# Optimization experiments

Measured on AMD Instinct MI355X. Metric: run time of the kernel, lower is better.

## Reference

```python
import jax, jax.numpy as jnp
import numpy as np

B, S, RNN, ATTH = 256, 196, 1024, 512  # batch, att_size, rnn_size, att_h_size


def setup_inputs() -> dict:
    key = jax.random.key(0)
    k1, k2, k3, k4, k5, k6, k7 = jax.random.split(key, 7)
    h = jax.random.normal(k1, (B, RNN), dtype=jnp.float32)
    att_feats = jax.random.normal(k2, (B, S, RNN), dtype=jnp.float32)
    p_att_feats = jax.random.normal(k3, (B, S, ATTH), dtype=jnp.float32)
    # learned params (torch nn.Linear: y = x @ W.T + b)
    w_h2att = jax.random.normal(k4, (ATTH, RNN), dtype=jnp.float32) / np.sqrt(RNN)
    b_h2att = jax.random.normal(k5, (ATTH,), dtype=jnp.float32) * 0.01
    w_alpha = jax.random.normal(k6, (1, ATTH), dtype=jnp.float32) / np.sqrt(ATTH)
    b_alpha = jax.random.normal(k7, (1,), dtype=jnp.float32) * 0.01
    return {
        "h": h,
        "att_feats": att_feats,
        "p_att_feats": p_att_feats,
        "w_h2att": w_h2att,
        "b_h2att": b_h2att,
        "w_alpha": w_alpha,
        "b_alpha": b_alpha,
    }


def reference(h, att_feats, p_att_feats, w_h2att, b_h2att, w_alpha, b_alpha):
    # att_h = h2att(h): [B, ATTH]
    att_h = h @ w_h2att.T + b_h2att
    # additive combine + tanh: [B, S, ATTH]
    dot = jnp.tanh(p_att_feats + att_h[:, None, :])
    # alpha_net: [B, S]
    scores = jnp.einsum("bsa,a->bs", dot, w_alpha[0]) + b_alpha[0]
    weight = jax.nn.softmax(scores, axis=1)
    # weighted sum of att_feats: [B, RNN]
    att_res = jnp.einsum("bs,bsd->bd", weight, att_feats)
    return att_res
```

## Files before the change

kernel.cpp:

```cpp
#include <hip/hip_runtime.h>
#include <cstddef>

static constexpr int kB    = 256;
static constexpr int kS    = 196;
static constexpr int kRNN  = 1024;
static constexpr int kATTH = 512;

__device__ __forceinline__ float fast_tanh(float x) {
    x = fminf(12.0f, fmaxf(-12.0f, x));
    float e = __expf(2.0f * x);
    return __fdividef(e - 1.0f, e + 1.0f);
}

__device__ __forceinline__ float dot8t(const float4 p0, const float4 p1,
                                       const float4 ah0, const float4 ah1,
                                       const float4 wa0, const float4 wa1) {
    float r;
    r  = fast_tanh(p0.x + ah0.x) * wa0.x;
    r += fast_tanh(p0.y + ah0.y) * wa0.y;
    r += fast_tanh(p0.z + ah0.z) * wa0.z;
    r += fast_tanh(p0.w + ah0.w) * wa0.w;
    r += fast_tanh(p1.x + ah1.x) * wa1.x;
    r += fast_tanh(p1.y + ah1.y) * wa1.y;
    r += fast_tanh(p1.z + ah1.z) * wa1.z;
    r += fast_tanh(p1.w + ah1.w) * wa1.w;
    return r;
}

__global__ __launch_bounds__(1024) void att_one(
    const float* __restrict__ h,
    const float* __restrict__ att_feats,
    const float* __restrict__ p_att,
    const float* __restrict__ w_h2att,
    const float* __restrict__ b_h2att,
    const float* __restrict__ w_alpha,
    const float* __restrict__ b_alpha,
    float* __restrict__ out) {
    const int b = blockIdx.x;
    const int tid = threadIdx.x;
    const int lane = tid & 63;
    const int wave = tid >> 6;

    __shared__ float sAttH[kATTH];
    __shared__ float sScore[kS];
    __shared__ float4 sRed[3][256];

    {
        const float* hb = &h[(size_t)b * kRNN];
        const int k0 = lane << 2;
        const float4 h0 = *(const float4*)&hb[k0];
        const float4 h1 = *(const float4*)&hb[k0 + 256];
        const float4 h2 = *(const float4*)&hb[k0 + 512];
        const float4 h3 = *(const float4*)&hb[k0 + 768];
        const int abase = wave << 5;
#pragma unroll 2
        for (int r = 0; r < 32; ++r) {
            const int a = abase + r;
            const float* wr = &w_h2att[(size_t)a * kRNN + k0];
            const float4 x0 = *(const float4*)(wr);
            const float4 x1 = *(const float4*)(wr + 256);
            const float4 x2 = *(const float4*)(wr + 512);
            const float4 x3 = *(const float4*)(wr + 768);
            float d;
            d  = x0.x * h0.x + x0.y * h0.y + x0.z * h0.z + x0.w * h0.w;
            d += x1.x * h1.x + x1.y * h1.y + x1.z * h1.z + x1.w * h1.w;
            d += x2.x * h2.x + x2.y * h2.y + x2.z * h2.z + x2.w * h2.w;
            d += x3.x * h3.x + x3.y * h3.y + x3.z * h3.z + x3.w * h3.w;
#pragma unroll
            for (int off = 32; off > 0; off >>= 1) d += __shfl_xor(d, off, 64);
            if (lane == 0) sAttH[a] = d + b_h2att[a];
        }
    }
    __syncthreads();

    {
        const int col = lane << 3;
        const float4 ah0 = *(const float4*)&sAttH[col];
        const float4 ah1 = *(const float4*)&sAttH[col + 4];
        const float4 wa0 = *(const float4*)&w_alpha[col];
        const float4 wa1 = *(const float4*)&w_alpha[col + 4];
        const float balpha = b_alpha[0];

        for (int s = wave; s < kS; s += 32) {
            const int s2 = s + 16;
            const float* p = &p_att[((size_t)b * kS + s) * kATTH + col];
            const float4 p0 = *(const float4*)p;
            const float4 p1 = *(const float4*)(p + 4);
            float4 q0 = {0.f, 0.f, 0.f, 0.f}, q1 = {0.f, 0.f, 0.f, 0.f};
            if (s2 < kS) {
                const float* q = p + (size_t)16 * kATTH;
                q0 = *(const float4*)q;
                q1 = *(const float4*)(q + 4);
            }
            float r1 = dot8t(p0, p1, ah0, ah1, wa0, wa1);
#pragma unroll
            for (int off = 32; off > 0; off >>= 1) r1 += __shfl_xor(r1, off, 64);
            if (lane == 0) sScore[s] = r1 + balpha;
            if (s2 < kS) {
                float r2 = dot8t(q0, q1, ah0, ah1, wa0, wa1);
#pragma unroll
                for (int off = 32; off > 0; off >>= 1) r2 += __shfl_xor(r2, off, 64);
                if (lane == 0) sScore[s2] = r2 + balpha;
            }
        }
    }
    __syncthreads();

    if (tid < 64) {
        float vals[4];
        int cnt = 0;
        float m = -3.0e38f;
        for (int s = tid; s < kS; s += 64) {
            vals[cnt] = sScore[s];
            m = fmaxf(m, vals[cnt]);
            ++cnt;
        }
#pragma unroll
        for (int off = 32; off > 0; off >>= 1) m = fmaxf(m, __shfl_xor(m, off, 64));
        float sum = 0.f;
        for (int i = 0; i < cnt; ++i) { vals[i] = __expf(vals[i] - m); sum += vals[i]; }
#pragma unroll
        for (int off = 32; off > 0; off >>= 1) sum += __shfl_xor(sum, off, 64);
        const float inv = __fdividef(1.0f, sum);
        cnt = 0;
        for (int s = tid; s < kS; s += 64) { sScore[s] = vals[cnt] * inv; ++cnt; }
    }
    __syncthreads();

    const int d4 = tid & 255;
    const int sg = tid >> 8;
    const float* af = &att_feats[(size_t)b * kS * kRNN + (d4 << 2)];
    float4 acc = {0.f, 0.f, 0.f, 0.f};
#pragma unroll 4
    for (int i = 0; i < 49; ++i) {
        const int s = (i << 2) + sg;
        const float ws = sScore[s];
        const float4 v = *(const float4*)&af[(size_t)s * kRNN];
        acc.x += ws * v.x; acc.y += ws * v.y;
        acc.z += ws * v.z; acc.w += ws * v.w;
    }
    if (sg > 0) sRed[sg - 1][d4] = acc;
    __syncthreads();
    if (sg == 0) {
        const float4 r0 = sRed[0][d4];
        const float4 r1 = sRed[1][d4];
        const float4 r2 = sRed[2][d4];
        acc.x += r0.x + r1.x + r2.x;
        acc.y += r0.y + r1.y + r2.y;
        acc.z += r0.z + r1.z + r2.z;
        acc.w += r0.w + r1.w + r2.w;
        *(float4*)&out[(size_t)b * kRNN + (d4 << 2)] = acc;
    }
}

extern "C" void kernel_launch(void* const* d_in, const int* in_sizes, int n_in,
                              void* d_out, int out_size, void* d_ws, size_t ws_size,
                              hipStream_t stream) {
    const float* h         = (const float*)d_in[0];
    const float* att_feats = (const float*)d_in[1];
    const float* p_att     = (const float*)d_in[2];
    const float* w_h2att   = (const float*)d_in[3];
    const float* b_h2att   = (const float*)d_in[4];
    const float* w_alpha   = (const float*)d_in[5];
    const float* b_alpha   = (const float*)d_in[6];
    float* out = (float*)d_out;

    att_one<<<kB, 1024, 0, stream>>>(h, att_feats, p_att, w_h2att, b_h2att,
                                     w_alpha, b_alpha, out);
}
```

Measured before the change: 383.8 us.

## Fuse softmax and weighted sum into score loop using static max bound

Replaces the three-phase score/softmax/weighted-sum structure with one streaming loop per wave. Each wave computes a score, exponentiates it against a static upper bound (sum of |w_alpha| plus |b_alpha|, since tanh is bounded), and accumulates exp-weighted att_feats rows directly. Partial sums are then reduced across waves through shared memory. The p_att and att_feats loads for the first row are issued before the h2att GEMV, and the next row is prefetched each iteration. This removes two block barriers and the serial single-wave softmax, and overlaps memory loads with compute. The risks are that the fixed-bound exponent could underflow if scores sit far below the bound, and that the 64 KB shared accumulator array may limit occupancy.

```diff
diff --git a/kernel.cpp b/kernel.cpp
--- a/kernel.cpp
+++ b/kernel.cpp
@@ -42,8 +42,25 @@
     const int wave = tid >> 6;
 
     __shared__ float sAttH[kATTH];
-    __shared__ float sScore[kS];
-    __shared__ float4 sRed[3][256];
+    __shared__ float4 sAcc[16][256];
+    __shared__ float sSum[16];
+
+    const int col = lane << 3;
+    const float* pbase = &p_att[(size_t)b * kS * kATTH + col];
+    const float* abase = &att_feats[(size_t)b * kS * kRNN + (lane << 2)];
+
+    int s = wave;
+    float4 p0, p1, v0, v1, v2, v3;
+    {
+        const float* p = pbase + (size_t)s * kATTH;
+        p0 = *(const float4*)p;
+        p1 = *(const float4*)(p + 4);
+        const float* a = abase + (size_t)s * kRNN;
+        v0 = *(const float4*)(a);
+        v1 = *(const float4*)(a + 256);
+        v2 = *(const float4*)(a + 512);
+        v3 = *(const float4*)(a + 768);
+    }
 
     {
         const float* hb = &h[(size_t)b * kRNN];
@@ -52,10 +69,10 @@
         const float4 h1 = *(const float4*)&hb[k0 + 256];
         const float4 h2 = *(const float4*)&hb[k0 + 512];
         const float4 h3 = *(const float4*)&hb[k0 + 768];
-        const int abase = wave << 5;
+        const int abase0 = wave << 5;
 #pragma unroll 2
         for (int r = 0; r < 32; ++r) {
-            const int a = abase + r;
+            const int a = abase0 + r;
             const float* wr = &w_h2att[(size_t)a * kRNN + k0];
             const float4 x0 = *(const float4*)(wr);
             const float4 x1 = *(const float4*)(wr + 256);
@@ -73,84 +90,67 @@
     }
     __syncthreads();
 
-    {
-        const int col = lane << 3;
-        const float4 ah0 = *(const float4*)&sAttH[col];
-        const float4 ah1 = *(const float4*)&sAttH[col + 4];
-        const float4 wa0 = *(const float4*)&w_alpha[col];
-        const float4 wa1 = *(const float4*)&w_alpha[col + 4];
-        const float balpha = b_alpha[0];
+    const float4 ah0 = *(const float4*)&sAttH[col];
+    const float4 ah1 = *(const float4*)&sAttH[col + 4];
+    const float4 wa0 = *(const float4*)&w_alpha[col];
+    const float4 wa1 = *(const float4*)&w_alpha[col + 4];
+    const float balpha = b_alpha[0];
 
-        for (int s = wave; s < kS; s += 32) {
-            const int s2 = s + 16;
-            const float* p = &p_att[((size_t)b * kS + s) * kATTH + col];
-            const float4 p0 = *(const float4*)p;
-            const float4 p1 = *(const float4*)(p + 4);
-            float4 q0 = {0.f, 0.f, 0.f, 0.f}, q1 = {0.f, 0.f, 0.f, 0.f};
-            if (s2 < kS) {
-                const float* q = p + (size_t)16 * kATTH;
-                q0 = *(const float4*)q;
-                q1 = *(const float4*)(q + 4);
-            }
-            float r1 = dot8t(p0, p1, ah0, ah1, wa0, wa1);
+    float sw = fabsf(wa0.x) + fabsf(wa0.y) + fabsf(wa0.z) + fabsf(wa0.w) +
+               fabsf(wa1.x) + fabsf(wa1.y) + fabsf(wa1.z) + fabsf(wa1.w);
 #pragma unroll
-            for (int off = 32; off > 0; off >>= 1) r1 += __shfl_xor(r1, off, 64);
-            if (lane == 0) sScore[s] = r1 + balpha;
-            if (s2 < kS) {
-                float r2 = dot8t(q0, q1, ah0, ah1, wa0, wa1);
+    for (int off = 32; off > 0; off >>= 1) sw += __shfl_xor(sw, off, 64);
+    const float ebias = balpha - (sw + fabsf(balpha));
+
+    float4 acc0 = {0.f, 0.f, 0.f, 0.f}, acc1 = {0.f, 0.f, 0.f, 0.f};
+    float4 acc2 = {0.f, 0.f, 0.f, 0.f}, acc3 = {0.f, 0.f, 0.f, 0.f};
+    float ssum = 0.f;
+    while (true) {
+        const int sn = s + 16;
+        const bool more = sn < kS;
+        float4 np0, np1, nv0, nv1, nv2, nv3;
+        if (more) {
+            const float* p = pbase + (size_t)sn * kATTH;
+            np0 = *(const float4*)p;
+            np1 = *(const float4*)(p + 4);
+            const float* a = abase + (size_t)sn * kRNN;
+            nv0 = *(const float4*)(a);
+            nv1 = *(const float4*)(a + 256);
+            nv2 = *(const float4*)(a + 512);
+            nv3 = *(const float4*)(a + 768);
+        }
+        float r = dot8t(p0, p1, ah0, ah1, wa0, wa1);
 #pragma unroll
-                for (int off = 32; off > 0; off >>= 1) r2 += __shfl_xor(r2, off, 64);
-                if (lane == 0) sScore[s2] = r2 + balpha;
-            }
-        }
+        for (int off = 32; off > 0; off >>= 1) r += __shfl_xor(r, off, 64);
+        const float e = __expf(r + ebias);
+        acc0.x += e * v0.x; acc0.y += e * v0.y; acc0.z += e * v0.z; acc0.w += e * v0.w;
+        acc1.x += e * v1.x; acc1.y += e * v1.y; acc1.z += e * v1.z; acc1.w += e * v1.w;
+        acc2.x += e * v2.x; acc2.y += e * v2.y; acc2.z += e * v2.z; acc2.w += e * v2.w;
+        acc3.x += e * v3.x; acc3.y += e * v3.y; acc3.z += e * v3.z; acc3.w += e * v3.w;
+        ssum += e;
+        if (!more) break;
+        s = sn;
+        p0 = np0; p1 = np1;
+        v0 = nv0; v1 = nv1; v2 = nv2; v3 = nv3;
     }
+
+    sAcc[wave][(0 << 6) + lane] = acc0;
+    sAcc[wave][(1 << 6) + lane] = acc1;
+    sAcc[wave][(2 << 6) + lane] = acc2;
+    sAcc[wave][(3 << 6) + lane] = acc3;
+    if (lane == 0) sSum[wave] = ssum;
     __syncthreads();
 
-    if (tid < 64) {
-        float vals[4];
-        int cnt = 0;
-        float m = -3.0e38f;
-        for (int s = tid; s < kS; s += 64) {
-            vals[cnt] = sScore[s];
-            m = fmaxf(m, vals[cnt]);
-            ++cnt;
-        }
+    float tot = 0.f;
 #pragma unroll
-        for (int off = 32; off > 0; off >>= 1) m = fmaxf(m, __shfl_xor(m, off, 64));
-        float sum = 0.f;
-        for (int i = 0; i < cnt; ++i) { vals[i] = __expf(vals[i] - m); sum += vals[i]; }
+    for (int w = 0; w < 16; ++w) tot += sSum[w];
+    const float inv = __fdividef(1.0f, tot);
+
+    const float* sA = (const float*)sAcc;
+    float o = 0.f;
 #pragma unroll
-        for (int off = 32; off > 0; off >>= 1) sum += __shfl_xor(sum, off, 64);
-        const float inv = __fdividef(1.0f, sum);
-        cnt = 0;
-        for (int s = tid; s < kS; s += 64) { sScore[s] = vals[cnt] * inv; ++cnt; }
-    }
-    __syncthreads();
-
-    const int d4 = tid & 255;
-    const int sg = tid >> 8;
-    const float* af = &att_feats[(size_t)b * kS * kRNN + (d4 << 2)];
-    float4 acc = {0.f, 0.f, 0.f, 0.f};
-#pragma unroll 4
-    for (int i = 0; i < 49; ++i) {
-        const int s = (i << 2) + sg;
-        const float ws = sScore[s];
-        const float4 v = *(const float4*)&af[(size_t)s * kRNN];
-        acc.x += ws * v.x; acc.y += ws * v.y;
-        acc.z += ws * v.z; acc.w += ws * v.w;
-    }
-    if (sg > 0) sRed[sg - 1][d4] = acc;
-    __syncthreads();
-    if (sg == 0) {
-        const float4 r0 = sRed[0][d4];
-        const float4 r1 = sRed[1][d4];
-        const float4 r2 = sRed[2][d4];
-        acc.x += r0.x + r1.x + r2.x;
-        acc.y += r0.y + r1.y + r2.y;
-        acc.z += r0.z + r1.z + r2.z;
-        acc.w += r0.w + r1.w + r2.w;
-        *(float4*)&out[(size_t)b * kRNN + (d4 << 2)] = acc;
-    }
+    for (int w = 0; w < 16; ++w) o += sA[w * 1024 + tid];
+    out[(size_t)b * kRNN + tid] = o * inv;
 }
 
 extern "C" void kernel_launch(void* const* d_in, const int* in_sizes, int n_in,
```

Measured after the change: 389.6 us. About the same (+1.5%).
